# Optimization experiments

Measured on AMD Instinct MI355X. Metric: run time of the kernel, lower is better.

Reference implementation:

```python
import jax, jax.numpy as jnp
import numpy as np

N_NODES = 100000
N_EDGES = 600000
D_FEAT = 128
N_OUT = 1


def setup_inputs() -> dict:
    key = jax.random.key(0)
    k1, k2, k3, k4 = jax.random.split(key, 4)
    node_inputs = jax.random.normal(k1, (N_NODES, D_FEAT), dtype=jnp.float32)
    r_indices = jax.random.randint(k2, (N_EDGES,), 0, N_NODES, dtype=jnp.int64)
    c_indices = jax.random.randint(k3, (N_EDGES,), 0, N_NODES, dtype=jnp.int64)
    w = jax.random.normal(k4, (D_FEAT, N_OUT), dtype=jnp.float32) * 0.05
    b = jnp.zeros((N_OUT,), dtype=jnp.float32)
    return {"node_inputs": node_inputs, "r_indices": r_indices,
            "c_indices": c_indices, "w": w, "b": b}


def reference(node_inputs, r_indices, c_indices, w, b):
    # Gather edge endpoints: [E, D]
    row_inputs = node_inputs[r_indices]
    col_inputs = node_inputs[c_indices]
    diff = jnp.abs(row_inputs - col_inputs)          # [E, D]
    out = diff @ w + b                               # [E, n_out]
    out = jnp.squeeze(out, axis=-1)                  # n_out == 1
    return out  # act is identity (default)
```

## Files before the change

kernel.cpp:

```cpp
#include <hip/hip_runtime.h>
#include <hip/hip_bf16.h>
#include <hip/hip_fp16.h>
#include <stdint.h>


#define D_FEAT 128

typedef _Float16 h2v __attribute__((ext_vector_type(2)));

__global__ __launch_bounds__(256) void convert_f32_to_f16(
    const float* __restrict__ src, __half* __restrict__ dst,
    const float* __restrict__ w, __half* __restrict__ wh, int n8)
{
    const int i = blockIdx.x * blockDim.x + threadIdx.x;

    if (blockIdx.x == 0 && threadIdx.x < (D_FEAT / 8)) {
        const float4* s = (const float4*)w + 2 * (size_t)threadIdx.x;
        const float4 a = s[0];
        const float4 c = s[1];
        float4 packed;
        ((__half2*)&packed)[0] = __floats2half2_rn(a.x, a.y);
        ((__half2*)&packed)[1] = __floats2half2_rn(a.z, a.w);
        ((__half2*)&packed)[2] = __floats2half2_rn(c.x, c.y);
        ((__half2*)&packed)[3] = __floats2half2_rn(c.z, c.w);
        ((float4*)wh)[threadIdx.x] = packed;
    }

    if (i >= n8) return;
    const float4* s = (const float4*)src + 2 * (size_t)i;
    const float4 a = s[0];
    const float4 c = s[1];
    float4 packed;
    ((__half2*)&packed)[0] = __floats2half2_rn(a.x, a.y);
    ((__half2*)&packed)[1] = __floats2half2_rn(a.z, a.w);
    ((__half2*)&packed)[2] = __floats2half2_rn(c.x, c.y);
    ((__half2*)&packed)[3] = __floats2half2_rn(c.z, c.w);
    ((float4*)dst)[i] = packed;
}

__device__ __forceinline__ float absdot(uint32_t a, uint32_t b, uint32_t w,
                                        float acc)
{
#if __has_builtin(__builtin_amdgcn_fdot2)
    const h2v av = __builtin_bit_cast(h2v, a);
    const h2v bv = __builtin_bit_cast(h2v, b);
    const h2v d  = av - bv;
    const uint32_t ad = __builtin_bit_cast(uint32_t, d) & 0x7FFF7FFFu;
    return __builtin_amdgcn_fdot2(__builtin_bit_cast(h2v, ad),
                                  __builtin_bit_cast(h2v, w), acc, false);
#else
    const float2 x = __half22float2(__builtin_bit_cast(__half2, a));
    const float2 y = __half22float2(__builtin_bit_cast(__half2, b));
    const float2 ww = __half22float2(__builtin_bit_cast(__half2, w));
    return acc + fabsf(x.x - y.x) * ww.x + fabsf(x.y - y.y) * ww.y;
#endif
}

__global__ __launch_bounds__(256) void gather_edges_f16_dot(
    const __half* __restrict__ tbl,
    const __half* __restrict__ wh,
    const int*   __restrict__ r_idx,
    const int*   __restrict__ c_idx,
    const float* __restrict__ b,
    float*       __restrict__ out,
    int n_edges)
{
    const int tid  = blockIdx.x * blockDim.x + threadIdx.x;
    const int lane = tid & 3;
    const int edge = tid >> 2;
    if (edge >= n_edges) return;

    const int r = r_idx[edge];
    const int c = c_idx[edge];

    const uint4* arow = (const uint4*)(tbl + (size_t)r * D_FEAT);
    const uint4* brow = (const uint4*)(tbl + (size_t)c * D_FEAT);

    const uint4 a0 = arow[lane];
    const uint4 a1 = arow[lane + 4];
    const uint4 a2 = arow[lane + 8];
    const uint4 a3 = arow[lane + 12];
    const uint4 b0 = brow[lane];
    const uint4 b1 = brow[lane + 4];
    const uint4 b2 = brow[lane + 8];
    const uint4 b3 = brow[lane + 12];

    const uint4* wv = (const uint4*)wh;
    const uint4 w0 = wv[lane];
    const uint4 w1 = wv[lane + 4];
    const uint4 w2 = wv[lane + 8];
    const uint4 w3 = wv[lane + 12];

    float s0 = 0.f, s1 = 0.f, s2 = 0.f, s3 = 0.f;
    s0 = absdot(a0.x, b0.x, w0.x, s0);
    s0 = absdot(a0.y, b0.y, w0.y, s0);
    s0 = absdot(a0.z, b0.z, w0.z, s0);
    s0 = absdot(a0.w, b0.w, w0.w, s0);

    s1 = absdot(a1.x, b1.x, w1.x, s1);
    s1 = absdot(a1.y, b1.y, w1.y, s1);
    s1 = absdot(a1.z, b1.z, w1.z, s1);
    s1 = absdot(a1.w, b1.w, w1.w, s1);

    s2 = absdot(a2.x, b2.x, w2.x, s2);
    s2 = absdot(a2.y, b2.y, w2.y, s2);
    s2 = absdot(a2.z, b2.z, w2.z, s2);
    s2 = absdot(a2.w, b2.w, w2.w, s2);

    s3 = absdot(a3.x, b3.x, w3.x, s3);
    s3 = absdot(a3.y, b3.y, w3.y, s3);
    s3 = absdot(a3.z, b3.z, w3.z, s3);
    s3 = absdot(a3.w, b3.w, w3.w, s3);

    float s = (s0 + s1) + (s2 + s3);

    s += __shfl_xor(s, 2, 64);
    s += __shfl_xor(s, 1, 64);

    if (lane == 0)
        out[edge] = s + b[0];
}

__global__ __launch_bounds__(256) void gather_edges_f32(
    const float* __restrict__ nodes,
    const int*   __restrict__ r_idx,
    const int*   __restrict__ c_idx,
    const float* __restrict__ w,
    const float* __restrict__ b,
    float*       __restrict__ out,
    int n_edges)
{
    const int tid  = blockIdx.x * blockDim.x + threadIdx.x;
    const int lane = tid & 31;
    const int edge = tid >> 5;
    if (edge >= n_edges) return;

    const int r = r_idx[edge];
    const int c = c_idx[edge];

    const float4 wv = ((const float4*)w)[lane];
    const float4 av = ((const float4*)(nodes + (size_t)r * D_FEAT))[lane];
    const float4 bv = ((const float4*)(nodes + (size_t)c * D_FEAT))[lane];

    float s = fabsf(av.x - bv.x) * wv.x
            + fabsf(av.y - bv.y) * wv.y
            + fabsf(av.z - bv.z) * wv.z
            + fabsf(av.w - bv.w) * wv.w;

    #pragma unroll
    for (int off = 16; off > 0; off >>= 1)
        s += __shfl_xor(s, off, 64);

    if (lane == 0)
        out[edge] = s + b[0];
}

extern "C" void kernel_launch(void* const* d_in, const int* in_sizes, int n_in,
                              void* d_out, int out_size, void* d_ws, size_t ws_size,
                              hipStream_t stream) {
    const float* nodes = (const float*)d_in[0];
    const int*   r_idx = (const int*)d_in[1];
    const int*   c_idx = (const int*)d_in[2];
    const float* w     = (const float*)d_in[3];
    const float* b     = (const float*)d_in[4];
    float*       out   = (float*)d_out;

    const int n_edges   = in_sizes[1];
    const int n_nodes_f = in_sizes[0];
    const size_t tbl_bytes = (size_t)n_nodes_f * sizeof(__half);
    const size_t wh_bytes  = (size_t)D_FEAT * sizeof(__half);

    if (ws_size >= tbl_bytes + wh_bytes && (n_nodes_f & 7) == 0) {
        __half* tbl = (__half*)d_ws;
        __half* wh  = tbl + (size_t)n_nodes_f;

        const int n8 = n_nodes_f / 8;
        const int cblock = 256;
        const int cgrid  = (n8 + cblock - 1) / cblock;
        convert_f32_to_f16<<<cgrid, cblock, 0, stream>>>(nodes, tbl, w, wh, n8);

        const int block = 256;
        const int grid  = (int)(((long long)n_edges * 4 + block - 1) / block);
        gather_edges_f16_dot<<<grid, block, 0, stream>>>(
            tbl, wh, r_idx, c_idx, b, out, n_edges);
    } else {
        const int block = 256;
        const int grid  = (int)(((long long)n_edges * 32 + block - 1) / block);
        gather_edges_f32<<<grid, block, 0, stream>>>(
            nodes, r_idx, c_idx, w, b, out, n_edges);
    }
}
```

Before: 130.2 us.

## Split fp16 node table into feature-block planes with partial-sum reduction

Measured after the change: 156.1 us. +19.9%, slower.

```diff
diff --git a/kernel.cpp b/kernel.cpp
--- a/kernel.cpp
+++ b/kernel.cpp
@@ -5,38 +5,10 @@
 
 
 #define D_FEAT 128
+#define DBLK   8
+#define DPB    16
 
 typedef _Float16 h2v __attribute__((ext_vector_type(2)));
-
-__global__ __launch_bounds__(256) void convert_f32_to_f16(
-    const float* __restrict__ src, __half* __restrict__ dst,
-    const float* __restrict__ w, __half* __restrict__ wh, int n8)
-{
-    const int i = blockIdx.x * blockDim.x + threadIdx.x;
-
-    if (blockIdx.x == 0 && threadIdx.x < (D_FEAT / 8)) {
-        const float4* s = (const float4*)w + 2 * (size_t)threadIdx.x;
-        const float4 a = s[0];
-        const float4 c = s[1];
-        float4 packed;
-        ((__half2*)&packed)[0] = __floats2half2_rn(a.x, a.y);
-        ((__half2*)&packed)[1] = __floats2half2_rn(a.z, a.w);
-        ((__half2*)&packed)[2] = __floats2half2_rn(c.x, c.y);
-        ((__half2*)&packed)[3] = __floats2half2_rn(c.z, c.w);
-        ((float4*)wh)[threadIdx.x] = packed;
-    }
-
-    if (i >= n8) return;
-    const float4* s = (const float4*)src + 2 * (size_t)i;
-    const float4 a = s[0];
-    const float4 c = s[1];
-    float4 packed;
-    ((__half2*)&packed)[0] = __floats2half2_rn(a.x, a.y);
-    ((__half2*)&packed)[1] = __floats2half2_rn(a.z, a.w);
-    ((__half2*)&packed)[2] = __floats2half2_rn(c.x, c.y);
-    ((__half2*)&packed)[3] = __floats2half2_rn(c.z, c.w);
-    ((float4*)dst)[i] = packed;
-}
 
 __device__ __forceinline__ float absdot(uint32_t a, uint32_t b, uint32_t w,
                                         float acc)
@@ -56,69 +28,115 @@
 #endif
 }
 
-__global__ __launch_bounds__(256) void gather_edges_f16_dot(
-    const __half* __restrict__ tbl,
+__global__ __launch_bounds__(256) void convert_transpose(
+    const float* __restrict__ src, __half* __restrict__ tbl2,
+    const float* __restrict__ w, __half* __restrict__ wh, int n_nodes)
+{
+    if (blockIdx.x == 0 && threadIdx.x < (D_FEAT / 8)) {
+        const float4* s = (const float4*)w + 2 * (size_t)threadIdx.x;
+        const float4 a = s[0];
+        const float4 c = s[1];
+        float4 packed;
+        ((__half2*)&packed)[0] = __floats2half2_rn(a.x, a.y);
+        ((__half2*)&packed)[1] = __floats2half2_rn(a.z, a.w);
+        ((__half2*)&packed)[2] = __floats2half2_rn(c.x, c.y);
+        ((__half2*)&packed)[3] = __floats2half2_rn(c.z, c.w);
+        ((float4*)wh)[threadIdx.x] = packed;
+    }
+
+    const int t = blockIdx.x * blockDim.x + threadIdx.x;
+    const int n = t >> 3;
+    const int k = t & (DBLK - 1);
+    if (n >= n_nodes) return;
+
+    const float4* s = (const float4*)(src + (size_t)n * D_FEAT + k * DPB);
+    const float4 f0 = s[0], f1 = s[1], f2 = s[2], f3 = s[3];
+    uint4 p0, p1;
+    __half2* h0 = (__half2*)&p0;
+    __half2* h1 = (__half2*)&p1;
+    h0[0] = __floats2half2_rn(f0.x, f0.y);
+    h0[1] = __floats2half2_rn(f0.z, f0.w);
+    h0[2] = __floats2half2_rn(f1.x, f1.y);
+    h0[3] = __floats2half2_rn(f1.z, f1.w);
+    h1[0] = __floats2half2_rn(f2.x, f2.y);
+    h1[1] = __floats2half2_rn(f2.z, f2.w);
+    h1[2] = __floats2half2_rn(f3.x, f3.y);
+    h1[3] = __floats2half2_rn(f3.z, f3.w);
+
+    uint4* d = (uint4*)(tbl2 + ((size_t)k * n_nodes + n) * DPB);
+    d[0] = p0;
+    d[1] = p1;
+}
+
+__global__ __launch_bounds__(256) void gather_partial(
+    const __half* __restrict__ tbl2,
     const __half* __restrict__ wh,
     const int*   __restrict__ r_idx,
     const int*   __restrict__ c_idx,
-    const float* __restrict__ b,
-    float*       __restrict__ out,
-    int n_edges)
-{
-    const int tid  = blockIdx.x * blockDim.x + threadIdx.x;
-    const int lane = tid & 3;
-    const int edge = tid >> 2;
-    if (edge >= n_edges) return;
-
-    const int r = r_idx[edge];
-    const int c = c_idx[edge];
-
-    const uint4* arow = (const uint4*)(tbl + (size_t)r * D_FEAT);
-    const uint4* brow = (const uint4*)(tbl + (size_t)c * D_FEAT);
-
-    const uint4 a0 = arow[lane];
-    const uint4 a1 = arow[lane + 4];
-    const uint4 a2 = arow[lane + 8];
-    const uint4 a3 = arow[lane + 12];
-    const uint4 b0 = brow[lane];
-    const uint4 b1 = brow[lane + 4];
-    const uint4 b2 = brow[lane + 8];
-    const uint4 b3 = brow[lane + 12];
-
-    const uint4* wv = (const uint4*)wh;
-    const uint4 w0 = wv[lane];
-    const uint4 w1 = wv[lane + 4];
-    const uint4 w2 = wv[lane + 8];
-    const uint4 w3 = wv[lane + 12];
-
-    float s0 = 0.f, s1 = 0.f, s2 = 0.f, s3 = 0.f;
+    float*       __restrict__ partial,
+    int n_edges, int n_nodes)
+{
+    const int dblk  = blockIdx.x & (DBLK - 1);
+    const int chunk = blockIdx.x >> 3;
+    const int e = chunk * blockDim.x + threadIdx.x;
+    if (e >= n_edges) return;
+
+    const int r = __builtin_nontemporal_load(r_idx + e);
+    const int c = __builtin_nontemporal_load(c_idx + e);
+
+    const __half* base = tbl2 + (size_t)dblk * n_nodes * DPB;
+    const uint4* rp = (const uint4*)(base + (size_t)r * DPB);
+    const uint4* cp = (const uint4*)(base + (size_t)c * DPB);
+
+    const uint4 a0 = rp[0];
+    const uint4 a1 = rp[1];
+    const uint4 b0 = cp[0];
+    const uint4 b1 = cp[1];
+
+    const uint4* wp = (const uint4*)(wh + dblk * DPB);
+    const uint4 w0 = wp[0];
+    const uint4 w1 = wp[1];
+
+    float s0 = 0.f, s1 = 0.f;
     s0 = absdot(a0.x, b0.x, w0.x, s0);
     s0 = absdot(a0.y, b0.y, w0.y, s0);
     s0 = absdot(a0.z, b0.z, w0.z, s0);
     s0 = absdot(a0.w, b0.w, w0.w, s0);
-
     s1 = absdot(a1.x, b1.x, w1.x, s1);
     s1 = absdot(a1.y, b1.y, w1.y, s1);
     s1 = absdot(a1.z, b1.z, w1.z, s1);
     s1 = absdot(a1.w, b1.w, w1.w, s1);
 
-    s2 = absdot(a2.x, b2.x, w2.x, s2);
-    s2 = absdot(a2.y, b2.y, w2.y, s2);
-    s2 = absdot(a2.z, b2.z, w2.z, s2);
-    s2 = absdot(a2.w, b2.w, w2.w, s2);
-
-    s3 = absdot(a3.x, b3.x, w3.x, s3);
-    s3 = absdot(a3.y, b3.y, w3.y, s3);
-    s3 = absdot(a3.z, b3.z, w3.z, s3);
-    s3 = absdot(a3.w, b3.w, w3.w, s3);
-
-    float s = (s0 + s1) + (s2 + s3);
-
-    s += __shfl_xor(s, 2, 64);
-    s += __shfl_xor(s, 1, 64);
-
-    if (lane == 0)
-        out[edge] = s + b[0];
+    __builtin_nontemporal_store(s0 + s1,
+                                partial + (size_t)dblk * n_edges + e);
+}
+
+__global__ __launch_bounds__(256) void reduce_partial(
+    const float* __restrict__ partial, const float* __restrict__ b,
+    float* __restrict__ out, int n_edges)
+{
+    const int q  = blockIdx.x * blockDim.x + threadIdx.x;
+    const int e0 = q * 4;
+    if (e0 >= n_edges) return;
+
+    if (e0 + 4 <= n_edges) {
+        const float bb = b[0];
+        float4 acc = make_float4(bb, bb, bb, bb);
+        #pragma unroll
+        for (int k = 0; k < DBLK; ++k) {
+            const float4 p =
+                *(const float4*)(partial + (size_t)k * n_edges + e0);
+            acc.x += p.x; acc.y += p.y; acc.z += p.z; acc.w += p.w;
+        }
+        *(float4*)(out + e0) = acc;
+    } else {
+        for (int e = e0; e < n_edges; ++e) {
+            float acc = b[0];
+            for (int k = 0; k < DBLK; ++k)
+                acc += partial[(size_t)k * n_edges + e];
+            out[e] = acc;
+        }
+    }
 }
 
 __global__ __launch_bounds__(256) void gather_edges_f32(
@@ -167,22 +185,39 @@
 
     const int n_edges   = in_sizes[1];
     const int n_nodes_f = in_sizes[0];
-    const size_t tbl_bytes = (size_t)n_nodes_f * sizeof(__half);
-    const size_t wh_bytes  = (size_t)D_FEAT * sizeof(__half);
-
-    if (ws_size >= tbl_bytes + wh_bytes && (n_nodes_f & 7) == 0) {
-        __half* tbl = (__half*)d_ws;
-        __half* wh  = tbl + (size_t)n_nodes_f;
-
-        const int n8 = n_nodes_f / 8;
-        const int cblock = 256;
-        const int cgrid  = (n8 + cblock - 1) / cblock;
-        convert_f32_to_f16<<<cgrid, cblock, 0, stream>>>(nodes, tbl, w, wh, n8);
-
-        const int block = 256;
-        const int grid  = (int)(((long long)n_edges * 4 + block - 1) / block);
-        gather_edges_f16_dot<<<grid, block, 0, stream>>>(
-            tbl, wh, r_idx, c_idx, b, out, n_edges);
+    const int n_nodes   = n_nodes_f / D_FEAT;
+
+    const size_t tbl_bytes  = (size_t)n_nodes_f * sizeof(__half);
+    const size_t wh_bytes   = (size_t)D_FEAT * sizeof(__half);
+    const size_t part_bytes = (size_t)DBLK * n_edges * sizeof(float);
+
+    if (ws_size >= tbl_bytes + wh_bytes + part_bytes &&
+        (n_nodes_f % D_FEAT) == 0) {
+        __half* tbl2    = (__half*)d_ws;
+        __half* wh      = tbl2 + (size_t)n_nodes_f;
+        float*  partial = (float*)((char*)d_ws + tbl_bytes + wh_bytes);
+
+        {
+            const int total = n_nodes * DBLK;
+            const int block = 256;
+            const int grid  = (total + block - 1) / block;
+            convert_transpose<<<grid, block, 0, stream>>>(
+                nodes, tbl2, w, wh, n_nodes);
+        }
+        {
+            const int block  = 256;
+            const int chunks = (n_edges + block - 1) / block;
+            const int grid   = chunks * DBLK;
+            gather_partial<<<grid, block, 0, stream>>>(
+                tbl2, wh, r_idx, c_idx, partial, n_edges, n_nodes);
+        }
+        {
+            const int block = 256;
+            const int quads = (n_edges + 3) / 4;
+            const int grid  = (quads + block - 1) / block;
+            reduce_partial<<<grid, block, 0, stream>>>(
+                partial, b, out, n_edges);
+        }
     } else {
         const int block = 256;
         const int grid  = (int)(((long long)n_edges * 32 + block - 1) / block);
```
